# Optimization experiments

Measured on AMD Instinct MI355X. Metric: run time of the kernel, lower is better.

Reference implementation:

```python
import jax, jax.numpy as jnp
import numpy as np

RATE = 0.1
INPUT_SHAPE = [8192]
BATCH_DIMS = 1
K = max(1, round(RATE * int(np.prod(INPUT_SHAPE))))  # 819


def setup_inputs() -> dict:
    key = jax.random.key(0)
    x = jax.random.normal(key, (4096, 8192), dtype=jnp.float32)
    return {"x": x}


def reference(x) -> jnp.ndarray:
    batch_flat = int(np.prod(x.shape[:BATCH_DIMS]))
    x_flat = x.reshape(batch_flat, -1)            # [B, D]
    ax = jnp.abs(x_flat)
    topk_vals, _ = jax.lax.top_k(ax, K)           # [B, K] sorted descending
    thr = topk_vals[:, -1:]                        # kth largest |x| per row
    mask = (ax >= thr).reshape(x.shape)
    return jnp.where(mask, x, jnp.zeros_like(x))
```

## Files before the change

kernel.cpp:

```cpp
#include <hip/hip_runtime.h>
#include <stdint.h>


constexpr int NCOLS = 8192;
constexpr int TPB   = 256;
constexpr int V4    = NCOLS / 4;
constexpr int VPT   = V4 / TPB;

constexpr int PAD = 8;
constexpr int B1 = 2048, C1 = 2;
constexpr int B2 = 1024, C2 = 4;
constexpr int S1 = B1 + PAD;
constexpr int S2 = B2 + PAD;
constexpr int HW = (C2 * S2 > C1 * S1) ? C2 * S2 : C1 * S1;

struct Shared {
  uint32_t hist[HW];
  uint32_t wavesum[4];
  uint32_t digit;
  uint32_t rem;
};

template <int BINS, int COPIES>
__device__ __forceinline__ uint32_t run_phase(Shared& sh, const uint4 (&v)[VPT],
                                              int dshift, int cshift, uint32_t cprefix,
                                              uint32_t& rem, int tid, int lane, int wave) {
  constexpr int BPT = BINS / TPB;
  constexpr int STRIDE = BINS + PAD;
  constexpr int ZW4 = (COPIES * STRIDE) / 4;

  uint4* hz = (uint4*)sh.hist;
  for (int i = tid; i < ZW4; i += TPB) hz[i] = make_uint4(0u, 0u, 0u, 0u);
  __syncthreads();

  uint32_t* h = &sh.hist[((wave * COPIES) >> 2) * STRIDE];
#pragma unroll
  for (int i = 0; i < VPT; ++i) {
    uint32_t a[4] = {v[i].x, v[i].y, v[i].z, v[i].w};
#pragma unroll
    for (int j = 0; j < 4; ++j) {
      uint32_t key = a[j] & 0x7fffffffu;
      if ((key >> cshift) == cprefix)
        atomicAdd(&h[(key >> dshift) & (BINS - 1)], 1u);
    }
  }
  __syncthreads();

  uint32_t hb[BPT];
#pragma unroll
  for (int j = 0; j < BPT; ++j) hb[j] = 0;
#pragma unroll
  for (int c = 0; c < COPIES; ++c) {
    const uint4* hp = (const uint4*)&sh.hist[c * STRIDE + tid * BPT];
#pragma unroll
    for (int q = 0; q < BPT / 4; ++q) {
      uint4 t = hp[q];
      hb[4 * q + 0] += t.x; hb[4 * q + 1] += t.y;
      hb[4 * q + 2] += t.z; hb[4 * q + 3] += t.w;
    }
  }
  uint32_t L = 0;
#pragma unroll
  for (int j = 0; j < BPT; ++j) L += hb[j];

  uint32_t suf = L;
#pragma unroll
  for (int off = 1; off < 64; off <<= 1) {
    uint32_t o = __shfl_down(suf, off, 64);
    suf += (lane + off < 64) ? o : 0u;
  }
  if (lane == 0) sh.wavesum[wave] = suf;
  __syncthreads();
  uint32_t addw = 0;
#pragma unroll
  for (int w = 0; w < 4; ++w) addw += (w > wave) ? sh.wavesum[w] : 0u;
  suf += addw;

  uint32_t s = suf - L;
#pragma unroll
  for (int j = BPT - 1; j >= 0; --j) {
    uint32_t snext = s;
    s += hb[j];
    if (s >= rem && snext < rem) {
      sh.digit = (uint32_t)(tid * BPT + j);
      sh.rem = rem - snext;
    }
  }
  __syncthreads();
  uint32_t d = sh.digit;
  rem = sh.rem;
  return d;
}

__global__ __launch_bounds__(TPB) void topk_row_kernel(const float* __restrict__ x,
                                                       float* __restrict__ out,
                                                       int K) {
  __shared__ Shared sh;
  const int row  = blockIdx.x;
  const int tid  = threadIdx.x;
  const int lane = tid & 63;
  const int wave = tid >> 6;

  const uint4* xr = (const uint4*)(x) + (size_t)row * V4;
  uint4 v[VPT];
#pragma unroll
  for (int i = 0; i < VPT; ++i) v[i] = xr[tid + i * TPB];

  uint32_t rem = (uint32_t)K;
  uint32_t d1 = run_phase<B1, C1>(sh, v, 20, 31, 0u, rem, tid, lane, wave);
  uint32_t d2 = run_phase<B2, C2>(sh, v, 10, 20, d1, rem, tid, lane, wave);
  uint32_t d3 = run_phase<B2, C2>(sh, v,  0, 10, (d1 << 10) | d2, rem, tid, lane, wave);

  const uint32_t thr = (d1 << 20) | (d2 << 10) | d3;

  uint4* outr = (uint4*)(out) + (size_t)row * V4;
#pragma unroll
  for (int i = 0; i < VPT; ++i) {
    uint4 o = v[i];
    o.x = ((o.x & 0x7fffffffu) >= thr) ? o.x : 0u;
    o.y = ((o.y & 0x7fffffffu) >= thr) ? o.y : 0u;
    o.z = ((o.z & 0x7fffffffu) >= thr) ? o.z : 0u;
    o.w = ((o.w & 0x7fffffffu) >= thr) ? o.w : 0u;
    outr[tid + i * TPB] = o;
  }
}

extern "C" void kernel_launch(void* const* d_in, const int* in_sizes, int n_in,
                              void* d_out, int out_size, void* d_ws, size_t ws_size,
                              hipStream_t stream) {
  (void)n_in; (void)out_size; (void)d_ws; (void)ws_size;
  const float* x = (const float*)d_in[0];
  float* out = (float*)d_out;
  const int rows = in_sizes[0] / NCOLS;
  const int K = (int)(0.1 * NCOLS + 0.5);
  topk_row_kernel<<<rows, TPB, 0, stream>>>(x, out, K);
}
```

Measured before the change: 230.2 us.

## Pack phase-1 histogram into 16-bit halves and shrink LDS for higher occupancy

```diff
diff --git a/kernel.cpp b/kernel.cpp
--- a/kernel.cpp
+++ b/kernel.cpp
@@ -8,11 +8,12 @@
 constexpr int VPT   = V4 / TPB;
 
 constexpr int PAD = 8;
-constexpr int B1 = 2048, C1 = 2;
-constexpr int B2 = 1024, C2 = 4;
-constexpr int S1 = B1 + PAD;
-constexpr int S2 = B2 + PAD;
-constexpr int HW = (C2 * S2 > C1 * S1) ? C2 * S2 : C1 * S1;
+constexpr int W1  = 1024;
+constexpr int S1  = W1 + PAD;
+constexpr int C1  = 2;
+constexpr int B2  = 1024;
+constexpr int S2  = B2 + PAD;
+constexpr int HW  = (C1 * S1 > S2) ? C1 * S1 : S2;
 
 struct Shared {
   uint32_t hist[HW];
@@ -21,44 +22,9 @@
   uint32_t rem;
 };
 
-template <int BINS, int COPIES>
-__device__ __forceinline__ uint32_t run_phase(Shared& sh, const uint4 (&v)[VPT],
-                                              int dshift, int cshift, uint32_t cprefix,
-                                              uint32_t& rem, int tid, int lane, int wave) {
-  constexpr int BPT = BINS / TPB;
-  constexpr int STRIDE = BINS + PAD;
-  constexpr int ZW4 = (COPIES * STRIDE) / 4;
-
-  uint4* hz = (uint4*)sh.hist;
-  for (int i = tid; i < ZW4; i += TPB) hz[i] = make_uint4(0u, 0u, 0u, 0u);
-  __syncthreads();
-
-  uint32_t* h = &sh.hist[((wave * COPIES) >> 2) * STRIDE];
-#pragma unroll
-  for (int i = 0; i < VPT; ++i) {
-    uint32_t a[4] = {v[i].x, v[i].y, v[i].z, v[i].w};
-#pragma unroll
-    for (int j = 0; j < 4; ++j) {
-      uint32_t key = a[j] & 0x7fffffffu;
-      if ((key >> cshift) == cprefix)
-        atomicAdd(&h[(key >> dshift) & (BINS - 1)], 1u);
-    }
-  }
-  __syncthreads();
-
-  uint32_t hb[BPT];
-#pragma unroll
-  for (int j = 0; j < BPT; ++j) hb[j] = 0;
-#pragma unroll
-  for (int c = 0; c < COPIES; ++c) {
-    const uint4* hp = (const uint4*)&sh.hist[c * STRIDE + tid * BPT];
-#pragma unroll
-    for (int q = 0; q < BPT / 4; ++q) {
-      uint4 t = hp[q];
-      hb[4 * q + 0] += t.x; hb[4 * q + 1] += t.y;
-      hb[4 * q + 2] += t.z; hb[4 * q + 3] += t.w;
-    }
-  }
+template <int BPT>
+__device__ __forceinline__ uint32_t pick_winner(Shared& sh, const uint32_t (&hb)[BPT],
+                                                uint32_t& rem, int tid, int lane, int wave) {
   uint32_t L = 0;
 #pragma unroll
   for (int j = 0; j < BPT; ++j) L += hb[j];
@@ -92,9 +58,76 @@
   return d;
 }
 
-__global__ __launch_bounds__(TPB) void topk_row_kernel(const float* __restrict__ x,
-                                                       float* __restrict__ out,
-                                                       int K) {
+__device__ __forceinline__ uint32_t phase1(Shared& sh, const uint4 (&v)[VPT],
+                                           uint32_t& rem, int tid, int lane, int wave) {
+  uint4* hz = (uint4*)sh.hist;
+  constexpr int ZW4 = (C1 * S1) / 4;
+  for (int i = tid; i < ZW4; i += TPB) hz[i] = make_uint4(0u, 0u, 0u, 0u);
+  __syncthreads();
+
+  uint32_t* h = &sh.hist[(wave >> 1) * S1];
+#pragma unroll
+  for (int i = 0; i < VPT; ++i) {
+    uint32_t a[4] = {v[i].x, v[i].y, v[i].z, v[i].w};
+#pragma unroll
+    for (int j = 0; j < 4; ++j) {
+      uint32_t d = (a[j] & 0x7fffffffu) >> 20;
+      atomicAdd(&h[d & (W1 - 1)], 1u << ((d >> 10) << 4));
+    }
+  }
+  __syncthreads();
+
+  constexpr int BPT = 2048 / TPB;
+  uint32_t hb[BPT];
+#pragma unroll
+  for (int j = 0; j < BPT; ++j) hb[j] = 0;
+  const int wbase = (tid & 127) * BPT;
+  const int shift = (tid >> 7) << 4;
+#pragma unroll
+  for (int c = 0; c < C1; ++c) {
+    const uint4* hp = (const uint4*)&sh.hist[c * S1 + wbase];
+#pragma unroll
+    for (int q = 0; q < BPT / 4; ++q) {
+      uint4 t = hp[q];
+      hb[4 * q + 0] += (t.x >> shift) & 0xffffu;
+      hb[4 * q + 1] += (t.y >> shift) & 0xffffu;
+      hb[4 * q + 2] += (t.z >> shift) & 0xffffu;
+      hb[4 * q + 3] += (t.w >> shift) & 0xffffu;
+    }
+  }
+  return pick_winner<BPT>(sh, hb, rem, tid, lane, wave);
+}
+
+__device__ __forceinline__ uint32_t phase23(Shared& sh, const uint4 (&v)[VPT],
+                                            int dshift, int cshift, uint32_t cprefix,
+                                            uint32_t& rem, int tid, int lane, int wave) {
+  uint4* hz = (uint4*)sh.hist;
+  constexpr int ZW4 = S2 / 4;
+  for (int i = tid; i < ZW4; i += TPB) hz[i] = make_uint4(0u, 0u, 0u, 0u);
+  __syncthreads();
+
+#pragma unroll
+  for (int i = 0; i < VPT; ++i) {
+    uint32_t a[4] = {v[i].x, v[i].y, v[i].z, v[i].w};
+#pragma unroll
+    for (int j = 0; j < 4; ++j) {
+      uint32_t key = a[j] & 0x7fffffffu;
+      if ((key >> cshift) == cprefix)
+        atomicAdd(&sh.hist[(key >> dshift) & (B2 - 1)], 1u);
+    }
+  }
+  __syncthreads();
+
+  constexpr int BPT = B2 / TPB;
+  uint32_t hb[BPT];
+  const uint4 t = *(const uint4*)&sh.hist[tid * BPT];
+  hb[0] = t.x; hb[1] = t.y; hb[2] = t.z; hb[3] = t.w;
+  return pick_winner<BPT>(sh, hb, rem, tid, lane, wave);
+}
+
+__global__ __launch_bounds__(TPB, 8) void topk_row_kernel(const float* __restrict__ x,
+                                                          float* __restrict__ out,
+                                                          int K) {
   __shared__ Shared sh;
   const int row  = blockIdx.x;
   const int tid  = threadIdx.x;
@@ -107,9 +140,9 @@
   for (int i = 0; i < VPT; ++i) v[i] = xr[tid + i * TPB];
 
   uint32_t rem = (uint32_t)K;
-  uint32_t d1 = run_phase<B1, C1>(sh, v, 20, 31, 0u, rem, tid, lane, wave);
-  uint32_t d2 = run_phase<B2, C2>(sh, v, 10, 20, d1, rem, tid, lane, wave);
-  uint32_t d3 = run_phase<B2, C2>(sh, v,  0, 10, (d1 << 10) | d2, rem, tid, lane, wave);
+  uint32_t d1 = phase1(sh, v, rem, tid, lane, wave);
+  uint32_t d2 = phase23(sh, v, 10, 20, d1, rem, tid, lane, wave);
+  uint32_t d3 = phase23(sh, v,  0, 10, (d1 << 10) | d2, rem, tid, lane, wave);
 
   const uint32_t thr = (d1 << 20) | (d2 << 10) | d3;
 
```

Measured after the change: 230.2 us. No clear change (+0.0%).

## Process one row per wavefront with wave-private histograms and ballot-based selection

Applied to the files above, without the earlier changes.

```diff
diff --git a/kernel.cpp b/kernel.cpp
--- a/kernel.cpp
+++ b/kernel.cpp
@@ -4,64 +4,43 @@
 
 constexpr int NCOLS = 8192;
 constexpr int TPB   = 256;
+constexpr int WAVES = TPB / 64;
 constexpr int V4    = NCOLS / 4;
-constexpr int VPT   = V4 / TPB;
+constexpr int VPL   = NCOLS / 64 / 4;
 
-constexpr int PAD = 8;
-constexpr int B1 = 2048, C1 = 2;
-constexpr int B2 = 1024, C2 = 4;
-constexpr int S1 = B1 + PAD;
-constexpr int S2 = B2 + PAD;
-constexpr int HW = (C2 * S2 > C1 * S1) ? C2 * S2 : C1 * S1;
+constexpr int WSTR   = 36;
+constexpr int HWORDS = WSTR * 64;
 
-struct Shared {
-  uint32_t hist[HW];
-  uint32_t wavesum[4];
-  uint32_t digit;
-  uint32_t rem;
-};
+__device__ __forceinline__ uint32_t bin_addr_p1(uint32_t d) {
+  return (uint32_t)WSTR * (d >> 5) + (d & 31u);
+}
+__device__ __forceinline__ uint32_t bin_addr_p23(uint32_t d) {
+  return (uint32_t)WSTR * (d >> 4) + (d & 15u);
+}
 
-template <int BINS, int COPIES>
-__device__ __forceinline__ uint32_t run_phase(Shared& sh, const uint4 (&v)[VPT],
-                                              int dshift, int cshift, uint32_t cprefix,
-                                              uint32_t& rem, int tid, int lane, int wave) {
-  constexpr int BPT = BINS / TPB;
-  constexpr int STRIDE = BINS + PAD;
-  constexpr int ZW4 = (COPIES * STRIDE) / 4;
+__device__ __forceinline__ void zero_hist(uint32_t* hist, int lane) {
+  uint4 z = make_uint4(0u, 0u, 0u, 0u);
+#pragma unroll
+  for (int j = 0; j < 8; ++j)
+    *(uint4*)&hist[4 * lane + 256 * j] = z;
+#pragma unroll
+  for (int j = 0; j < 4; ++j)
+    hist[2048 + 64 * j + lane] = 0u;
+}
 
-  uint4* hz = (uint4*)sh.hist;
-  for (int i = tid; i < ZW4; i += TPB) hz[i] = make_uint4(0u, 0u, 0u, 0u);
-  __syncthreads();
-
-  uint32_t* h = &sh.hist[((wave * COPIES) >> 2) * STRIDE];
+template <int BPL>
+__device__ __forceinline__ uint32_t scan_pick(const uint32_t* hist, uint32_t& rem,
+                                              int lane) {
+  uint32_t c[BPL];
 #pragma unroll
-  for (int i = 0; i < VPT; ++i) {
-    uint32_t a[4] = {v[i].x, v[i].y, v[i].z, v[i].w};
-#pragma unroll
-    for (int j = 0; j < 4; ++j) {
-      uint32_t key = a[j] & 0x7fffffffu;
-      if ((key >> cshift) == cprefix)
-        atomicAdd(&h[(key >> dshift) & (BINS - 1)], 1u);
-    }
-  }
-  __syncthreads();
-
-  uint32_t hb[BPT];
-#pragma unroll
-  for (int j = 0; j < BPT; ++j) hb[j] = 0;
-#pragma unroll
-  for (int c = 0; c < COPIES; ++c) {
-    const uint4* hp = (const uint4*)&sh.hist[c * STRIDE + tid * BPT];
-#pragma unroll
-    for (int q = 0; q < BPT / 4; ++q) {
-      uint4 t = hp[q];
-      hb[4 * q + 0] += t.x; hb[4 * q + 1] += t.y;
-      hb[4 * q + 2] += t.z; hb[4 * q + 3] += t.w;
-    }
+  for (int j = 0; j < BPL / 4; ++j) {
+    uint4 t = *(const uint4*)&hist[WSTR * lane + 4 * j];
+    c[4 * j + 0] = t.x; c[4 * j + 1] = t.y;
+    c[4 * j + 2] = t.z; c[4 * j + 3] = t.w;
   }
   uint32_t L = 0;
 #pragma unroll
-  for (int j = 0; j < BPT; ++j) L += hb[j];
+  for (int j = 0; j < BPL; ++j) L += c[j];
 
   uint32_t suf = L;
 #pragma unroll
@@ -69,59 +48,91 @@
     uint32_t o = __shfl_down(suf, off, 64);
     suf += (lane + off < 64) ? o : 0u;
   }
-  if (lane == 0) sh.wavesum[wave] = suf;
-  __syncthreads();
-  uint32_t addw = 0;
-#pragma unroll
-  for (int w = 0; w < 4; ++w) addw += (w > wave) ? sh.wavesum[w] : 0u;
-  suf += addw;
 
   uint32_t s = suf - L;
+  bool won = false;
+  uint32_t wd = 0, wr = 0;
 #pragma unroll
-  for (int j = BPT - 1; j >= 0; --j) {
+  for (int j = BPL - 1; j >= 0; --j) {
     uint32_t snext = s;
-    s += hb[j];
+    s += c[j];
     if (s >= rem && snext < rem) {
-      sh.digit = (uint32_t)(tid * BPT + j);
-      sh.rem = rem - snext;
+      won = true;
+      wd = (uint32_t)(lane * BPL + j);
+      wr = rem - snext;
     }
   }
-  __syncthreads();
-  uint32_t d = sh.digit;
-  rem = sh.rem;
-  return d;
+  uint64_t m = __ballot(won);
+  int owner = __ffsll((unsigned long long)m) - 1;
+  rem = (uint32_t)__shfl((int)wr, owner, 64);
+  return (uint32_t)__shfl((int)wd, owner, 64);
 }
 
-__global__ __launch_bounds__(TPB) void topk_row_kernel(const float* __restrict__ x,
-                                                       float* __restrict__ out,
-                                                       int K) {
-  __shared__ Shared sh;
-  const int row  = blockIdx.x;
+__device__ __forceinline__ uint32_t phase23(uint32_t* hist, const uint4 (&v)[VPL],
+                                            int dshift, int cshift, uint32_t cprefix,
+                                            uint32_t& rem, int lane) {
+  zero_hist(hist, lane);
+  __threadfence_block();
+#pragma unroll
+  for (int j = 0; j < VPL; ++j) {
+    uint32_t a[4] = {v[j].x, v[j].y, v[j].z, v[j].w};
+#pragma unroll
+    for (int q = 0; q < 4; ++q) {
+      uint32_t key = a[q] & 0x7fffffffu;
+      if ((key >> cshift) == cprefix)
+        atomicAdd(&hist[bin_addr_p23((key >> dshift) & 1023u)], 1u);
+    }
+  }
+  __threadfence_block();
+  return scan_pick<16>(hist, rem, lane);
+}
+
+__global__ __launch_bounds__(TPB, 2) void topk_row_kernel(const float* __restrict__ x,
+                                                          float* __restrict__ out,
+                                                          int K, int nrows) {
+  __shared__ uint32_t histAll[WAVES * HWORDS];
   const int tid  = threadIdx.x;
   const int lane = tid & 63;
   const int wave = tid >> 6;
+  const int row  = blockIdx.x * WAVES + wave;
+  if (row >= nrows) return;
 
+  uint32_t* hist = &histAll[wave * HWORDS];
   const uint4* xr = (const uint4*)(x) + (size_t)row * V4;
-  uint4 v[VPT];
+
+  uint4 v[VPL];
 #pragma unroll
-  for (int i = 0; i < VPT; ++i) v[i] = xr[tid + i * TPB];
+  for (int j = 0; j < VPL; ++j) v[j] = xr[lane + 64 * j];
 
+  zero_hist(hist, lane);
+  __threadfence_block();
+#pragma unroll
+  for (int j = 0; j < VPL; ++j) {
+    uint32_t a[4] = {v[j].x, v[j].y, v[j].z, v[j].w};
+#pragma unroll
+    for (int q = 0; q < 4; ++q) {
+      uint32_t d = (a[q] & 0x7fffffffu) >> 20;
+      atomicAdd(&hist[bin_addr_p1(d)], 1u);
+    }
+  }
+  __threadfence_block();
   uint32_t rem = (uint32_t)K;
-  uint32_t d1 = run_phase<B1, C1>(sh, v, 20, 31, 0u, rem, tid, lane, wave);
-  uint32_t d2 = run_phase<B2, C2>(sh, v, 10, 20, d1, rem, tid, lane, wave);
-  uint32_t d3 = run_phase<B2, C2>(sh, v,  0, 10, (d1 << 10) | d2, rem, tid, lane, wave);
+  uint32_t d1 = scan_pick<32>(hist, rem, lane);
+
+  uint32_t d2 = phase23(hist, v, 10, 20, d1, rem, lane);
+  uint32_t d3 = phase23(hist, v, 0, 10, (d1 << 10) | d2, rem, lane);
 
   const uint32_t thr = (d1 << 20) | (d2 << 10) | d3;
 
   uint4* outr = (uint4*)(out) + (size_t)row * V4;
 #pragma unroll
-  for (int i = 0; i < VPT; ++i) {
-    uint4 o = v[i];
+  for (int j = 0; j < VPL; ++j) {
+    uint4 o = v[j];
     o.x = ((o.x & 0x7fffffffu) >= thr) ? o.x : 0u;
     o.y = ((o.y & 0x7fffffffu) >= thr) ? o.y : 0u;
     o.z = ((o.z & 0x7fffffffu) >= thr) ? o.z : 0u;
     o.w = ((o.w & 0x7fffffffu) >= thr) ? o.w : 0u;
-    outr[tid + i * TPB] = o;
+    outr[lane + 64 * j] = o;
   }
 }
 
@@ -133,5 +144,6 @@
   float* out = (float*)d_out;
   const int rows = in_sizes[0] / NCOLS;
   const int K = (int)(0.1 * NCOLS + 0.5);
-  topk_row_kernel<<<rows, TPB, 0, stream>>>(x, out, K);
+  const int grid = (rows + WAVES - 1) / WAVES;
+  topk_row_kernel<<<grid, TPB, 0, stream>>>(x, out, K, rows);
 }
```

New measurement: 241.9 us. 1.05x slower.
